# Kernel tuning notes

Measured on AMD Instinct MI355X. Metric: run time of the kernel, lower is better.

The kernel has to match this reference:

```python
import jax, jax.numpy as jnp
from jax import lax
import numpy as np

N, T, PD, TD, F, E, GB = 2048, 256, 5, 5, 128, 65536, 5


def _lstm_layer(x, Wih, Whh, bih, bhh):
    # x: [B, T, D] -> [B, T, H], torch LSTM gate order (i, f, g, o)
    B = x.shape[0]
    H = Whh.shape[1]
    b = bih + bhh

    def step(carry, xt):
        h, c = carry
        gates = xt @ Wih.T + h @ Whh.T + b
        i, f, g, o = jnp.split(gates, 4, axis=-1)
        c = jax.nn.sigmoid(f) * c + jax.nn.sigmoid(i) * jnp.tanh(g)
        h = jax.nn.sigmoid(o) * jnp.tanh(c)
        return (h, c), h

    h0 = jnp.zeros((B, H), x.dtype)
    _, hs = lax.scan(step, (h0, h0), jnp.swapaxes(x, 0, 1))
    return jnp.swapaxes(hs, 0, 1)


def _attention(x, W1, b1, W2, b2):
    # Fused prefix (cumulative causal) softmax attention.
    # Original loops over t computing softmax(scores[:, :t+1]); here:
    # ctx[t] = cumsum(e * x)[t] / cumsum(e)[t] with a global max shift
    # (softmax is shift-invariant, so this equals the per-prefix softmax).
    s = (jnp.tanh(x @ W1.T + b1) @ W2.T + b2)[..., 0]  # [B, T]
    e = jnp.exp(s - jnp.max(s, axis=1, keepdims=True))  # [B, T]
    num = jnp.cumsum(e[..., None] * x, axis=1)          # [B, T, D]
    den = jnp.cumsum(e, axis=1)[..., None]              # [B, T, 1]
    return jnp.sum(num / den, axis=1)                   # [B, D]


def _gcn(x, W, b, edge_index, edge_weight):
    # PyG GCNConv with normalize=True: add self-loops (w=1), symmetric norm.
    n = x.shape[0]
    loop = jnp.arange(n)
    row = jnp.concatenate([edge_index[0], loop])
    col = jnp.concatenate([edge_index[1], loop])
    w = jnp.concatenate([edge_weight, jnp.ones((n,), edge_weight.dtype)])
    deg = jax.ops.segment_sum(w, col, num_segments=n)
    dinv = jnp.where(deg > 0, deg ** -0.5, 0.0)
    norm = dinv[row] * w * dinv[col]
    h = x @ W.T
    out = jax.ops.segment_sum(norm[:, None] * h[row], col, num_segments=n)
    return out + b


def _forward(price, global_trend, p_weights, t_weights,
             lp_Wih0, lp_Whh0, lp_bih0, lp_bhh0, lp_Wih1, lp_Whh1, lp_bih1, lp_bhh1,
             lt_Wih0, lt_Whh0, lt_bih0, lt_bhh0, lt_Wih1, lt_Whh1, lt_bih1, lt_bhh1,
             ap_W1, ap_b1, ap_W2, ap_b2, at_W1, at_b1, at_W2, at_b2,
             gp1_W, gp1_b, gp2_W, gp2_b, gt1_W, gt1_b, gt2_W, gt2_b,
             mlp_W, mlp_b, p_edge_index, t_edge_index):
    x = _lstm_layer(price, lp_Wih0, lp_Whh0, lp_bih0, lp_bhh0)
    x = _lstm_layer(x, lp_Wih1, lp_Whh1, lp_bih1, lp_bhh1)
    x = _attention(x, ap_W1, ap_b1, ap_W2, ap_b2)            # [N, F]
    g = _lstm_layer(global_trend, lt_Wih0, lt_Whh0, lt_bih0, lt_bhh0)
    g = _lstm_layer(g, lt_Wih1, lt_Whh1, lt_bih1, lt_bhh1)
    g = _attention(g, at_W1, at_b1, at_W2, at_b2)            # [GB, F]
    pg = _gcn(x, gp1_W, gp1_b, p_edge_index, p_weights)
    pg = _gcn(pg, gp2_W, gp2_b, p_edge_index, p_weights)     # [N, F]
    # NOTE: original feeds x (not g) into the trend graph convs.
    tg = _gcn(x, gt1_W, gt1_b, t_edge_index, t_weights)
    tg = _gcn(tg, gt2_W, gt2_b, t_edge_index, t_weights)     # [N, F]
    trend = tg @ g.T                                         # [N, GB]
    feat = jnp.concatenate([pg, trend], axis=1)              # [N, F+GB]
    return jax.nn.sigmoid(feat @ mlp_W.T + mlp_b)            # [N, 1]


def setup_inputs() -> dict:
    key = jax.random.key(0)
    ks = iter(jax.random.split(key, 64))
    nrm = lambda shape, s=0.05: jax.random.normal(next(ks), shape, jnp.float32) * s
    inp = {}
    inp['price'] = jax.random.normal(next(ks), (N, T, PD), jnp.float32)
    inp['global_trend'] = jax.random.normal(next(ks), (GB, T, TD), jnp.float32)
    inp['p_edge_index'] = jax.random.randint(next(ks), (2, E), 0, N)
    inp['p_weights'] = jax.random.uniform(next(ks), (E,), jnp.float32)
    inp['t_edge_index'] = jax.random.randint(next(ks), (2, E), 0, N)
    inp['t_weights'] = jax.random.uniform(next(ks), (E,), jnp.float32)
    for pre, d in (('lp', PD), ('lt', TD)):
        inp[pre + '_Wih0'] = nrm((4 * F, d)); inp[pre + '_Whh0'] = nrm((4 * F, F))
        inp[pre + '_bih0'] = nrm((4 * F,));   inp[pre + '_bhh0'] = nrm((4 * F,))
        inp[pre + '_Wih1'] = nrm((4 * F, F)); inp[pre + '_Whh1'] = nrm((4 * F, F))
        inp[pre + '_bih1'] = nrm((4 * F,));   inp[pre + '_bhh1'] = nrm((4 * F,))
    for pre in ('ap', 'at'):
        inp[pre + '_W1'] = nrm((F, F)); inp[pre + '_b1'] = jnp.zeros((F,), jnp.float32)
        inp[pre + '_W2'] = nrm((1, F)); inp[pre + '_b2'] = jnp.zeros((1,), jnp.float32)
    for pre in ('gp', 'gt'):
        inp[pre + '1_W'] = nrm((16, F)); inp[pre + '1_b'] = jnp.zeros((16,), jnp.float32)
        inp[pre + '2_W'] = nrm((F, 16)); inp[pre + '2_b'] = jnp.zeros((F,), jnp.float32)
    inp['mlp_W'] = nrm((1, F + GB)); inp['mlp_b'] = jnp.zeros((1,), jnp.float32)
    return inp


def reference(price, global_trend, p_edge_index, p_weights, t_edge_index, t_weights,
              lp_Wih0, lp_Whh0, lp_bih0, lp_bhh0, lp_Wih1, lp_Whh1, lp_bih1, lp_bhh1,
              lt_Wih0, lt_Whh0, lt_bih0, lt_bhh0, lt_Wih1, lt_Whh1, lt_bih1, lt_bhh1,
              ap_W1, ap_b1, ap_W2, ap_b2, at_W1, at_b1, at_W2, at_b2,
              gp1_W, gp1_b, gp2_W, gp2_b, gt1_W, gt1_b, gt2_W, gt2_b,
              mlp_W, mlp_b):
    return _forward(price, global_trend, p_weights, t_weights,
                    lp_Wih0, lp_Whh0, lp_bih0, lp_bhh0, lp_Wih1, lp_Whh1, lp_bih1, lp_bhh1,
                    lt_Wih0, lt_Whh0, lt_bih0, lt_bhh0, lt_Wih1, lt_Whh1, lt_bih1, lt_bhh1,
                    ap_W1, ap_b1, ap_W2, ap_b2, at_W1, at_b1, at_W2, at_b2,
                    gp1_W, gp1_b, gp2_W, gp2_b, gt1_W, gt1_b, gt2_W, gt2_b,
                    mlp_W, mlp_b, p_edge_index, t_edge_index)
```

## Files before the change

kernel.cpp:

```cpp
#include <hip/hip_runtime.h>
#include <hip/hip_bf16.h>
#include <cstddef>

#define TT    256
#define NROW  2048
#define GBN   5
#define EDG   65536

using f32x4  = __attribute__((ext_vector_type(4))) float;
using bf16x8 = __attribute__((ext_vector_type(8))) short;

__device__ __forceinline__ void pinv(bf16x8& x) { asm volatile("" : "+v"(x)); }

__device__ __forceinline__ void barrier_lgkm() {
  asm volatile("s_waitcnt lgkmcnt(0)" ::: "memory");
  __builtin_amdgcn_s_barrier();
}

__device__ __forceinline__ float exp2fa(float x) { float r; asm("v_exp_f32 %0, %1" : "=v"(r) : "v"(x)); return r; }
__device__ __forceinline__ float rcpfa(float x)  { float r; asm("v_rcp_f32 %0, %1" : "=v"(r) : "v"(x)); return r; }
#define L2E 1.4426950408889634f
__device__ __forceinline__ float sigf(float x) { return rcpfa(1.0f + exp2fa(x * -L2E)); }
__device__ __forceinline__ float tanh_fast(float x) {
  float t = exp2fa(x * (-2.0f * L2E));
  return (1.0f - t) * rcpfa(1.0f + t);
}

enum : int {
  XBUF   = 425984,
  GBUFO  = 688128,
  DINVP  = 688768,
  DINVT  = 690816,
  H16    = 692864,
  PG1    = 725632,
  H128   = 758400,
  PGB    = 1020544,
  TG1    = 1282688,
  TGB    = 1315456,
  WS_END = 1577600
};

enum : int {
  N_P0   = 0,
  N_P1I  = 65536,
  N_P1H  = 131072,
  N_PA   = 196608,
  N_T0   = 212992,
  N_T1I  = 278528,
  N_T1H  = 344064,
  N_TA   = 409600
};

enum : long long {
  C0S_O   = 1577600,
  C1S_O   = 1841792,
  H1IMG_O = 2105984,
  SMST_O  = 2370176,
  NUMS_O  = 2374304,
  ACCOS_O = 2638496,
  H0S_O   = 2902688
};

struct SmemPipe {
  ushort a[2][2048];
  ushort b[2][2048];
  float  x[2560];
  float  s[2][8][16];
};

__global__ void k_pack(const float* __restrict__ Wa, const float* __restrict__ Wb,
                       int K1, int K2, int NT, int KS, ushort* __restrict__ dst) {
  int t = blockIdx.x * blockDim.x + threadIdx.x;
  int total = KS * NT * 2 * 64;
  if (t >= total) return;
  int lane = t & 63;
  int part = (t >> 6) & 1;
  int rest = t >> 7;
  int nt = rest % NT, kk = rest / NT;
  int j = nt * 16 + (lane & 15);
  int kbase = kk * 32 + (lane >> 4) * 8;
  bf16x8 o;
  #pragma unroll
  for (int e = 0; e < 8; ++e) {
    int k = kbase + e;
    float x = (k < K1) ? Wa[(size_t)j * K1 + k] : Wb[(size_t)j * K2 + (k - K1)];
    __hip_bfloat16 hi = __float2bfloat16(x);
    ushort u;
    if (part == 0) {
      u = *(ushort*)&hi;
    } else {
      float lo = x - __bfloat162float(hi);
      __hip_bfloat16 lob = __float2bfloat16(lo);
      u = *(ushort*)&lob;
    }
    o[e] = (short)u;
  }
  ((bf16x8*)dst)[t] = o;
}

__global__ void k_zero(float* __restrict__ p, int n) {
  int i = blockIdx.x * blockDim.x + threadIdx.x;
  if (i < n) p[i] = 0.0f;
}
__global__ void k_fill1(float* __restrict__ p, int n) {
  int i = blockIdx.x * blockDim.x + threadIdx.x;
  if (i < n) p[i] = 1.0f;
}
__global__ void k_deg(const int* __restrict__ col, const float* __restrict__ w,
                      float* __restrict__ deg, int n) {
  int i = blockIdx.x * blockDim.x + threadIdx.x;
  if (i < n) atomicAdd(&deg[col[i]], w[i]);
}
__global__ void k_dinv(float* __restrict__ deg, int n) {
  int i = blockIdx.x * blockDim.x + threadIdx.x;
  if (i < n) deg[i] = rsqrtf(deg[i]);
}

__device__ static void lstm0_body(
    SmemPipe* sm, int b,
    const float* __restrict__ price, const float* __restrict__ gtrend,
    const float* __restrict__ ws_ro, ushort* __restrict__ h0S, float* __restrict__ c0S,
    const float* __restrict__ Wih0p, const float* __restrict__ bi0p, const float* __restrict__ bh0p,
    const float* __restrict__ Wih0t, const float* __restrict__ bi0t, const float* __restrict__ bh0t,
    int nPrice, int t0, int TCp, int first)
{
  const int tid = threadIdx.x;
  const int w = tid >> 6, l = tid & 63;
  const int lq = l >> 4, lr = l & 15;
  const int rb = lq * 4;
  const int kcol = w * 16 + lr;
  const bool isP = b < nPrice;
  const int R = isP ? 16 : GBN;
  const float* seq = isP ? (price + (size_t)b * 16 * (TT * 5)) : gtrend;
  const ushort* S0 = (const ushort*)(ws_ro + (isP ? N_P0 : N_T0));
  const float* Wih0 = isP ? Wih0p : Wih0t;
  const float* bi0 = isP ? bi0p : bi0t;
  const float* bh0 = isP ? bh0p : bh0t;

  auto h0hi = sm->a;
  auto h0lo = sm->b;
  float* xsa = sm->x;

  bf16x8 wh[4][4], wl[4][4];
  #pragma unroll
  for (int kk = 0; kk < 4; ++kk)
    #pragma unroll
    for (int g = 0; g < 4; ++g) {
      int blk = (kk * 32 + (w + 8 * g)) * 2;
      wh[kk][g] = ((const bf16x8*)S0)[(blk + 0) * 64 + l];
      wl[kk][g] = ((const bf16x8*)S0)[(blk + 1) * 64 + l];
      pinv(wh[kk][g]); pinv(wl[kk][g]);
    }
  float wih0r[4][5], bg0[4];
  #pragma unroll
  for (int g = 0; g < 4; ++g) {
    int j = kcol + 128 * g;
    bg0[g] = bi0[j] + bh0[j];
    #pragma unroll
    for (int k = 0; k < 5; ++k) wih0r[g][k] = Wih0[j * 5 + k];
  }

  const size_t bstr = (size_t)b * (size_t)TCp * 4096;
  float c0[4] = {0, 0, 0, 0};

  for (int i = tid; i < TCp * 80; i += 512) {
    int tl = i / 80, rem = i % 80, r = rem / 5, k = rem % 5;
    xsa[tl * 80 + rem] = (r < R) ? seq[(size_t)r * (TT * 5) + (size_t)(t0 + tl) * 5 + k] : 0.0f;
  }
  if (first) {
    for (int i = tid; i < 2048; i += 512) { h0hi[0][i] = 0; h0lo[0][i] = 0; }
  } else {
    const size_t lb = bstr + (size_t)(TCp - 1) * 4096;
    *(uint2*)&h0hi[0][4 * tid] = *(const uint2*)&h0S[lb + 4 * tid];
    *(uint2*)&h0lo[0][4 * tid] = *(const uint2*)&h0S[lb + 2048 + 4 * tid];
    #pragma unroll
    for (int reg = 0; reg < 4; ++reg)
      c0[reg] = c0S[(size_t)b * 2048 + (size_t)(rb + reg) * 128 + kcol];
  }
  __syncthreads();

  const int kkhi = (kcol >> 3) & 3;
  const int eo = kcol & 7;
  const int b0w = rb + 16 * kkhi;
  const int kkw = kcol >> 5;
  int wro[4];
  #pragma unroll
  for (int reg = 0; reg < 4; ++reg) wro[reg] = kkw * 512 + (b0w + (reg ^ lq)) * 8 + eo;
  const int rdo = (l ^ ((l >> 2) & 3)) * 8;

  int cur = 0;
  for (int tl = 0; tl < TCp; ++tl) {
    const int nxt = cur ^ 1;
    if (tl > 0) {
      *(uint2*)&h0S[bstr + (size_t)(tl - 1) * 4096 + 4 * tid] = *(const uint2*)&h0hi[cur][4 * tid];
      *(uint2*)&h0S[bstr + (size_t)(tl - 1) * 4096 + 2048 + 4 * tid] = *(const uint2*)&h0lo[cur][4 * tid];
    }

    f32x4 acc[4];
    #pragma unroll
    for (int g = 0; g < 4; ++g) acc[g] = (f32x4){bg0[g], bg0[g], bg0[g], bg0[g]};
    #pragma unroll
    for (int k = 0; k < 5; ++k) {
      float xv[4];
      #pragma unroll
      for (int reg = 0; reg < 4; ++reg) xv[reg] = xsa[tl * 80 + (rb + reg) * 5 + k];
      #pragma unroll
      for (int g = 0; g < 4; ++g)
        #pragma unroll
        for (int reg = 0; reg < 4; ++reg)
          acc[g][reg] = fmaf(xv[reg], wih0r[g][k], acc[g][reg]);
    }
    #pragma unroll
    for (int kk = 0; kk < 4; ++kk) {
      bf16x8 ah = *(const bf16x8*)&h0hi[cur][kk * 512 + rdo];
      bf16x8 al = *(const bf16x8*)&h0lo[cur][kk * 512 + rdo];
      #pragma unroll
      for (int g = 0; g < 4; ++g) {
        acc[g] = __builtin_amdgcn_mfma_f32_16x16x32_bf16(ah, wh[kk][g], acc[g], 0, 0, 0);
        acc[g] = __builtin_amdgcn_mfma_f32_16x16x32_bf16(al, wh[kk][g], acc[g], 0, 0, 0);
        acc[g] = __builtin_amdgcn_mfma_f32_16x16x32_bf16(ah, wl[kk][g], acc[g], 0, 0, 0);
      }
    }
    #pragma unroll
    for (int reg = 0; reg < 4; ++reg) {
      float gi = acc[0][reg], gf = acc[1][reg], gg = acc[2][reg], go = acc[3][reg];
      float c = sigf(gf) * c0[reg] + sigf(gi) * tanh_fast(gg);
      c0[reg] = c;
      float h = sigf(go) * tanh_fast(c);
      __hip_bfloat16 hb = __float2bfloat16(h);
      float lo = h - __bfloat162float(hb);
      __hip_bfloat16 lb = __float2bfloat16(lo);
      h0hi[nxt][wro[reg]] = *(ushort*)&hb;
      h0lo[nxt][wro[reg]] = *(ushort*)&lb;
    }
    barrier_lgkm();
    cur = nxt;
  }
  *(uint2*)&h0S[bstr + (size_t)(TCp - 1) * 4096 + 4 * tid] = *(const uint2*)&h0hi[cur][4 * tid];
  *(uint2*)&h0S[bstr + (size_t)(TCp - 1) * 4096 + 2048 + 4 * tid] = *(const uint2*)&h0lo[cur][4 * tid];

  #pragma unroll
  for (int reg = 0; reg < 4; ++reg)
    c0S[(size_t)b * 2048 + (size_t)(rb + reg) * 128 + kcol] = c0[reg];
}

__device__ static void lstm1_body(
    SmemPipe* sm, int b,
    const float* __restrict__ pre1, const float* __restrict__ ws_ro,
    float* __restrict__ xout, float* __restrict__ gout,
    float* __restrict__ c1S, ushort* __restrict__ h1imgS, float* __restrict__ smS,
    float* __restrict__ numS, float* __restrict__ accOS,
    const float* __restrict__ apB1, const float* __restrict__ apW2, const float* __restrict__ apB2,
    const float* __restrict__ atB1, const float* __restrict__ atW2, const float* __restrict__ atB2,
    int nPrice, int TCp, int first)
{
  const int tid = threadIdx.x;
  const int w = tid >> 6, l = tid & 63;
  const int lq = l >> 4, lr = l & 15;
  const int rb = lq * 4;
  const int kcol = w * 16 + lr;
  const bool isP = b < nPrice;
  const int R = isP ? 16 : GBN;
  const ushort* S1H = (const ushort*)(ws_ro + (isP ? N_P1H : N_T1H));
  const ushort* SA  = (const ushort*)(ws_ro + (isP ? N_PA : N_TA));
  const float* b1ap = isP ? apB1 : atB1;
  const float* w2p  = isP ? apW2 : atW2;
  const float  b2v  = isP ? apB2[0] : atB2[0];

  auto h1hi = sm->a;
  auto h1lo = sm->b;
  auto sbuf = sm->s;

  bf16x8 hh[4][4], hl[4][4];
  #pragma unroll
  for (int kk = 0; kk < 4; ++kk)
    #pragma unroll
    for (int g = 0; g < 4; ++g) {
      int blk = (kk * 32 + (w + 8 * g)) * 2;
      hh[kk][g] = ((const bf16x8*)S1H)[(blk + 0) * 64 + l];
      hl[kk][g] = ((const bf16x8*)S1H)[(blk + 1) * 64 + l];
      pinv(hh[kk][g]); pinv(hl[kk][g]);
    }
  bf16x8 wa[4], wal[4];
  #pragma unroll
  for (int kk = 0; kk < 4; ++kk) {
    wa[kk]  = ((const bf16x8*)SA)[((kk * 8 + w) * 2 + 0) * 64 + l];
    wal[kk] = ((const bf16x8*)SA)[((kk * 8 + w) * 2 + 1) * 64 + l];
    pinv(wa[kk]); pinv(wal[kk]);
  }
  const float w2r = w2p[kcol], b1ar = b1ap[kcol];

  float c1[4] = {0, 0, 0, 0}, h1r[4] = {0, 0, 0, 0}, h1r_prev[4];
  float num[4] = {0, 0, 0, 0}, accO[4] = {0, 0, 0, 0};
  float m_run[4], den_r[4];

  if (first) {
    for (int i = tid; i < 2048; i += 512) { h1hi[0][i] = 0; h1lo[0][i] = 0; }
    #pragma unroll
    for (int reg = 0; reg < 4; ++reg) { m_run[reg] = -1e30f; den_r[reg] = 0.0f; }
  } else {
    const size_t ib = (size_t)b * 4096;
    *(uint2*)&h1hi[0][4 * tid] = *(const uint2*)&h1imgS[ib + 4 * tid];
    *(uint2*)&h1lo[0][4 * tid] = *(const uint2*)&h1imgS[ib + 2048 + 4 * tid];
    const size_t sb = (size_t)b * 2048;
    #pragma unroll
    for (int reg = 0; reg < 4; ++reg) {
      size_t o = sb + (size_t)(rb + reg) * 128 + kcol;
      c1[reg] = c1S[o];
      num[reg] = numS[o];
      accO[reg] = accOS[o];
      m_run[reg] = smS[(size_t)b * 32 + (size_t)(rb + reg) * 2];
      den_r[reg] = smS[(size_t)b * 32 + (size_t)(rb + reg) * 2 + 1];
    }
  }
  __syncthreads();

  const int kkhi = (kcol >> 3) & 3;
  const int eo = kcol & 7;
  const int b0w = rb + 16 * kkhi;
  const int kkw = kcol >> 5;
  int wro[4];
  #pragma unroll
  for (int reg = 0; reg < 4; ++reg) wro[reg] = kkw * 512 + (b0w + (reg ^ lq)) * 8 + eo;
  const int rdo = (l ^ ((l >> 2) & 3)) * 8;

  const float* pbase = pre1 + (size_t)b * TCp * 8192 + (size_t)tid * 16;

  f32x4 pnext[4];
  #pragma unroll
  for (int g = 0; g < 4; ++g) pnext[g] = *(const f32x4*)&pbase[g * 4];

  int cur = 0;
  for (int tl = 0; tl < TCp; ++tl) {
    const int nxt = cur ^ 1;
    f32x4 acc[4];
    #pragma unroll
    for (int g = 0; g < 4; ++g) acc[g] = pnext[g];
    if (tl + 1 < TCp) {
      #pragma unroll
      for (int g = 0; g < 4; ++g)
        pnext[g] = *(const f32x4*)&pbase[(size_t)(tl + 1) * 8192 + g * 4];
    }

    #pragma unroll
    for (int kk = 0; kk < 4; ++kk) {
      bf16x8 ah = *(const bf16x8*)&h1hi[cur][kk * 512 + rdo];
      bf16x8 al = *(const bf16x8*)&h1lo[cur][kk * 512 + rdo];
      #pragma unroll
      for (int g = 0; g < 4; ++g) {
        acc[g] = __builtin_amdgcn_mfma_f32_16x16x32_bf16(ah, hh[kk][g], acc[g], 0, 0, 0);
        acc[g] = __builtin_amdgcn_mfma_f32_16x16x32_bf16(al, hh[kk][g], acc[g], 0, 0, 0);
        acc[g] = __builtin_amdgcn_mfma_f32_16x16x32_bf16(ah, hl[kk][g], acc[g], 0, 0, 0);
      }
    }
    #pragma unroll
    for (int reg = 0; reg < 4; ++reg) {
      h1r_prev[reg] = h1r[reg];
      float gi = acc[0][reg], gf = acc[1][reg], gg = acc[2][reg], go = acc[3][reg];
      float c = sigf(gf) * c1[reg] + sigf(gi) * tanh_fast(gg);
      c1[reg] = c;
      float h = sigf(go) * tanh_fast(c);
      h1r[reg] = h;
      __hip_bfloat16 hb = __float2bfloat16(h);
      float lo = h - __bfloat162float(hb);
      __hip_bfloat16 lb = __float2bfloat16(lo);
      h1hi[nxt][wro[reg]] = *(ushort*)&hb;
      h1lo[nxt][wro[reg]] = *(ushort*)&lb;
    }
    barrier_lgkm();

    if (tl > 0) {
      const int pb = (tl - 1) & 1;
      #pragma unroll
      for (int reg = 0; reg < 4; ++reg) {
        float s = b2v;
        #pragma unroll
        for (int ww = 0; ww < 8; ++ww) s += sbuf[pb][ww][rb + reg];
        float m0 = m_run[reg];
        float nm = fmaxf(m0, s);
        float e = exp2fa((s - nm) * L2E), sc = exp2fa((m0 - nm) * L2E);
        float d = den_r[reg] * sc + e;
        m_run[reg] = nm; den_r[reg] = d;
        num[reg] = num[reg] * sc + e * h1r_prev[reg];
        accO[reg] = fmaf(num[reg], rcpfa(d), accO[reg]);
      }
    }

    f32x4 aa = (f32x4){b1ar, b1ar, b1ar, b1ar};
    #pragma unroll
    for (int kk = 0; kk < 4; ++kk) {
      bf16x8 ah = *(const bf16x8*)&h1hi[nxt][kk * 512 + rdo];
      bf16x8 al = *(const bf16x8*)&h1lo[nxt][kk * 512 + rdo];
      aa = __builtin_amdgcn_mfma_f32_16x16x32_bf16(ah, wa[kk], aa, 0, 0, 0);
      aa = __builtin_amdgcn_mfma_f32_16x16x32_bf16(al, wa[kk], aa, 0, 0, 0);
      aa = __builtin_amdgcn_mfma_f32_16x16x32_bf16(ah, wal[kk], aa, 0, 0, 0);
    }
    float p[4];
    #pragma unroll
    for (int reg = 0; reg < 4; ++reg) p[reg] = tanh_fast(aa[reg]) * w2r;
    #pragma unroll
    for (int m = 1; m < 16; m <<= 1) {
      #pragma unroll
      for (int reg = 0; reg < 4; ++reg) p[reg] += __shfl_xor(p[reg], m);
    }
    if (lr == 0) {
      #pragma unroll
      for (int reg = 0; reg < 4; ++reg) sbuf[tl & 1][w][rb + reg] = p[reg];
    }
    cur = nxt;
  }
  barrier_lgkm();
  {
    const int pb = (TCp - 1) & 1;
    #pragma unroll
    for (int reg = 0; reg < 4; ++reg) {
      float s = b2v;
      #pragma unroll
      for (int ww = 0; ww < 8; ++ww) s += sbuf[pb][ww][rb + reg];
      float m0 = m_run[reg];
      float nm = fmaxf(m0, s);
      float e = exp2fa((s - nm) * L2E), sc = exp2fa((m0 - nm) * L2E);
      float d = den_r[reg] * sc + e;
      m_run[reg] = nm; den_r[reg] = d;
      num[reg] = num[reg] * sc + e * h1r[reg];
      accO[reg] = fmaf(num[reg], rcpfa(d), accO[reg]);
    }
  }

  {
    const size_t ib = (size_t)b * 4096;
    *(uint2*)&h1imgS[ib + 4 * tid] = *(const uint2*)&h1hi[cur][4 * tid];
    *(uint2*)&h1imgS[ib + 2048 + 4 * tid] = *(const uint2*)&h1lo[cur][4 * tid];
    const size_t sb = (size_t)b * 2048;
    #pragma unroll
    for (int reg = 0; reg < 4; ++reg) {
      size_t o = sb + (size_t)(rb + reg) * 128 + kcol;
      c1S[o] = c1[reg];
      numS[o] = num[reg];
      accOS[o] = accO[reg];
    }
    if (w == 0 && lr == 0) {
      #pragma unroll
      for (int reg = 0; reg < 4; ++reg) {
        smS[(size_t)b * 32 + (size_t)(rb + reg) * 2] = m_run[reg];
        smS[(size_t)b * 32 + (size_t)(rb + reg) * 2 + 1] = den_r[reg];
      }
    }
  }

  float* dstx = isP ? (xout + (size_t)b * 16 * 128) : gout;
  #pragma unroll
  for (int reg = 0; reg < 4; ++reg) {
    int r = rb + reg;
    if (r < R) dstx[(size_t)r * 128 + kcol] = accO[reg];
  }
}

__global__ __launch_bounds__(512, 2) void k_pipe(
    const float* __restrict__ price, const float* __restrict__ gtrend,
    const float* __restrict__ ws_ro, ushort* __restrict__ h0S, float* __restrict__ c0S,
    const float* __restrict__ Wih0p, const float* __restrict__ bi0p, const float* __restrict__ bh0p,
    const float* __restrict__ Wih0t, const float* __restrict__ bi0t, const float* __restrict__ bh0t,
    const float* __restrict__ pre1,
    float* __restrict__ xout, float* __restrict__ gout,
    float* __restrict__ c1S, ushort* __restrict__ h1imgS, float* __restrict__ smS,
    float* __restrict__ numS, float* __restrict__ accOS,
    const float* __restrict__ apB1, const float* __restrict__ apW2, const float* __restrict__ apB2,
    const float* __restrict__ atB1, const float* __restrict__ atW2, const float* __restrict__ atB2,
    int nPrice, int t0A, int TCp, int firstA, int firstB, int doA, int doB)
{
  __shared__ SmemPipe sm;
  const int bid = blockIdx.x;
  if (bid < 129) {
    if (doA)
      lstm0_body(&sm, bid, price, gtrend, ws_ro, h0S, c0S,
                 Wih0p, bi0p, bh0p, Wih0t, bi0t, bh0t, nPrice, t0A, TCp, firstA);
  } else {
    if (doB)
      lstm1_body(&sm, bid - 129, pre1, ws_ro, xout, gout,
                 c1S, h1imgS, smS, numS, accOS,
                 apB1, apW2, apB2, atB1, atW2, atB2, nPrice, TCp, firstB);
  }
}

__global__ __launch_bounds__(512, 2) void k_pre1(
    const ushort* __restrict__ h0S, const float* __restrict__ ws_ro,
    float* __restrict__ pre1,
    const float* __restrict__ bi1p, const float* __restrict__ bh1p,
    const float* __restrict__ bi1t, const float* __restrict__ bh1t,
    int nPrice, int TCp, int nsub)
{
  const int b = blockIdx.x / nsub, sub = blockIdx.x % nsub;
  const int tid = threadIdx.x;
  const int w = tid >> 6, l = tid & 63;
  const int lr = l & 15;
  const int kcol = w * 16 + lr;
  const bool isP = b < nPrice;
  const ushort* S1I = (const ushort*)(ws_ro + (isP ? N_P1I : N_T1I));
  const float* bi1 = isP ? bi1p : bi1t;
  const float* bh1 = isP ? bh1p : bh1t;
  float bg1[4];
  #pragma unroll
  for (int g = 0; g < 4; ++g) bg1[g] = bi1[kcol + 128 * g] + bh1[kcol + 128 * g];
  const int rdo = (l ^ ((l >> 2) & 3)) * 8;
  const size_t bstr = (size_t)b * (size_t)TCp * 4096;
  const int t0 = sub * 4;

  f32x4 acc[4][4];
  #pragma unroll
  for (int ts = 0; ts < 4; ++ts)
    #pragma unroll
    for (int g = 0; g < 4; ++g) acc[ts][g] = (f32x4){bg1[g], bg1[g], bg1[g], bg1[g]};

  #pragma unroll
  for (int kk = 0; kk < 4; ++kk) {
    bf16x8 bh_[4], bl_[4];
    #pragma unroll
    for (int g = 0; g < 4; ++g) {
      int blk = (kk * 32 + (w + 8 * g)) * 2;
      bh_[g] = ((const bf16x8*)S1I)[(blk + 0) * 64 + l];
      bl_[g] = ((const bf16x8*)S1I)[(blk + 1) * 64 + l];
    }
    #pragma unroll
    for (int ts = 0; ts < 4; ++ts) {
      const size_t tb = bstr + (size_t)(t0 + ts) * 4096 + kk * 512 + rdo;
      bf16x8 ah = *(const bf16x8*)&h0S[tb];
      bf16x8 al = *(const bf16x8*)&h0S[tb + 2048];
      #pragma unroll
      for (int g = 0; g < 4; ++g) {
        acc[ts][g] = __builtin_amdgcn_mfma_f32_16x16x32_bf16(ah, bh_[g], acc[ts][g], 0, 0, 0);
        acc[ts][g] = __builtin_amdgcn_mfma_f32_16x16x32_bf16(al, bh_[g], acc[ts][g], 0, 0, 0);
        acc[ts][g] = __builtin_amdgcn_mfma_f32_16x16x32_bf16(ah, bl_[g], acc[ts][g], 0, 0, 0);
      }
    }
  }
  #pragma unroll
  for (int ts = 0; ts < 4; ++ts)
    #pragma unroll
    for (int g = 0; g < 4; ++g)
      *(f32x4*)&pre1[((size_t)b * TCp + (t0 + ts)) * 8192 + (size_t)tid * 16 + g * 4] = acc[ts][g];
}

__global__ void k_lin(const float* __restrict__ x, const float* __restrict__ W,
                      float* __restrict__ h, int M, int K, int n) {
  int i = blockIdx.x * blockDim.x + threadIdx.x;
  if (i >= n) return;
  int r = i / M, m = i % M;
  const float* xr = x + (size_t)r * K;
  const float* wm = W + (size_t)m * K;
  float a = 0.f;
  for (int k = 0; k < K; ++k) a = fmaf(xr[k], wm[k], a);
  h[i] = a;
}

__global__ void k_scatter(const int* __restrict__ rowi, const int* __restrict__ coli,
                          const float* __restrict__ w, const float* __restrict__ dinv,
                          const float* __restrict__ h, float* __restrict__ outp,
                          int M, long long n) {
  long long i = (long long)blockIdx.x * blockDim.x + threadIdx.x;
  if (i >= n) return;
  int e = (int)(i / M), f = (int)(i % M);
  int rs = rowi[e], cd = coli[e];
  float nrm = dinv[rs] * w[e] * dinv[cd];
  atomicAdd(&outp[(size_t)cd * M + f], nrm * h[(size_t)rs * M + f]);
}

__global__ void k_gcn_fin(float* __restrict__ io, const float* __restrict__ h,
                          const float* __restrict__ dinv, const float* __restrict__ b,
                          int M, int n) {
  int i = blockIdx.x * blockDim.x + threadIdx.x;
  if (i >= n) return;
  int v = i / M, f = i % M;
  float dv = dinv[v];
  io[i] += dv * dv * h[i] + b[f];
}

__global__ __launch_bounds__(256) void k_final(const float* __restrict__ pg, const float* __restrict__ tg,
                                               const float* __restrict__ g, const float* __restrict__ mw,
                                               const float* __restrict__ mb, float* __restrict__ outp) {
  int wv = threadIdx.x >> 6, ln = threadIdx.x & 63;
  int r = blockIdx.x * 4 + wv;
  const float* pr = pg + (size_t)r * 128;
  const float* tr = tg + (size_t)r * 128;
  float pa = pr[ln] * mw[ln] + pr[ln + 64] * mw[ln + 64];
  float t0 = tr[ln], t1 = tr[ln + 64];
  float s[GBN];
  #pragma unroll
  for (int gb = 0; gb < GBN; ++gb)
    s[gb] = g[gb * 128 + ln] * t0 + g[gb * 128 + 64 + ln] * t1;
  #pragma unroll
  for (int o = 32; o > 0; o >>= 1) {
    pa += __shfl_down(pa, o);
    #pragma unroll
    for (int gb = 0; gb < GBN; ++gb) s[gb] += __shfl_down(s[gb], o);
  }
  if (ln == 0) {
    float lg = pa + mb[0];
    #pragma unroll
    for (int gb = 0; gb < GBN; ++gb) lg = fmaf(s[gb], mw[128 + gb], lg);
    outp[r] = 1.0f / (1.0f + __expf(-lg));
  }
}

static inline int gdiv(long long n) { return (int)((n + 255) / 256); }

extern "C" void kernel_launch(void* const* d_in, const int* in_sizes, int n_in,
                              void* d_out, int out_size, void* d_ws, size_t ws_size,
                              hipStream_t stream) {
  const float* price  = (const float*)d_in[0];
  const float* gtrend = (const float*)d_in[1];
  const int*   p_ei   = (const int*)d_in[2];
  const float* p_w    = (const float*)d_in[3];
  const int*   t_ei   = (const int*)d_in[4];
  const float* t_w    = (const float*)d_in[5];
  const float* lpWih0 = (const float*)d_in[6];
  const float* lpWhh0 = (const float*)d_in[7];
  const float* lpBih0 = (const float*)d_in[8];
  const float* lpBhh0 = (const float*)d_in[9];
  const float* lpWih1 = (const float*)d_in[10];
  const float* lpWhh1 = (const float*)d_in[11];
  const float* lpBih1 = (const float*)d_in[12];
  const float* lpBhh1 = (const float*)d_in[13];
  const float* ltWih0 = (const float*)d_in[14];
  const float* ltWhh0 = (const float*)d_in[15];
  const float* ltBih0 = (const float*)d_in[16];
  const float* ltBhh0 = (const float*)d_in[17];
  const float* ltWih1 = (const float*)d_in[18];
  const float* ltWhh1 = (const float*)d_in[19];
  const float* ltBih1 = (const float*)d_in[20];
  const float* ltBhh1 = (const float*)d_in[21];
  const float* apW1 = (const float*)d_in[22];
  const float* apB1 = (const float*)d_in[23];
  const float* apW2 = (const float*)d_in[24];
  const float* apB2 = (const float*)d_in[25];
  const float* atW1 = (const float*)d_in[26];
  const float* atB1 = (const float*)d_in[27];
  const float* atW2 = (const float*)d_in[28];
  const float* atB2 = (const float*)d_in[29];
  const float* gp1W = (const float*)d_in[30];
  const float* gp1b = (const float*)d_in[31];
  const float* gp2W = (const float*)d_in[32];
  const float* gp2b = (const float*)d_in[33];
  const float* gt1W = (const float*)d_in[34];
  const float* gt1b = (const float*)d_in[35];
  const float* gt2W = (const float*)d_in[36];
  const float* gt2b = (const float*)d_in[37];
  const float* mlpW = (const float*)d_in[38];
  const float* mlpb = (const float*)d_in[39];

  float* ws = (float*)d_ws;
  float* outp = (float*)d_out;
  if (ws_size < (size_t)WS_END * sizeof(float)) return;

  int TC = 0;
  for (int cand = 32; cand >= 8; cand >>= 1) {
    unsigned long long need = ((unsigned long long)H0S_O + 129ULL * cand * (2048ULL + 8192ULL)) * 4ULL;
    if ((unsigned long long)ws_size >= need) { TC = cand; break; }
  }
  if (TC == 0) return;

  k_pack<<<gdiv(16384), 256, 0, stream>>>(lpWhh0, lpWhh0, 128, 128, 32, 4, (ushort*)(ws + N_P0));
  k_pack<<<gdiv(16384), 256, 0, stream>>>(lpWih1, lpWih1, 128, 128, 32, 4, (ushort*)(ws + N_P1I));
  k_pack<<<gdiv(16384), 256, 0, stream>>>(lpWhh1, lpWhh1, 128, 128, 32, 4, (ushort*)(ws + N_P1H));
  k_pack<<<gdiv(4096),  256, 0, stream>>>(apW1,   apW1,   128, 128,  8, 4, (ushort*)(ws + N_PA));
  k_pack<<<gdiv(16384), 256, 0, stream>>>(ltWhh0, ltWhh0, 128, 128, 32, 4, (ushort*)(ws + N_T0));
  k_pack<<<gdiv(16384), 256, 0, stream>>>(ltWih1, ltWih1, 128, 128, 32, 4, (ushort*)(ws + N_T1I));
  k_pack<<<gdiv(16384), 256, 0, stream>>>(ltWhh1, ltWhh1, 128, 128, 32, 4, (ushort*)(ws + N_T1H));
  k_pack<<<gdiv(4096),  256, 0, stream>>>(atW1,   atW1,   128, 128,  8, 4, (ushort*)(ws + N_TA));

  k_fill1<<<gdiv(NROW), 256, 0, stream>>>(ws + DINVP, NROW);
  k_deg<<<gdiv(EDG), 256, 0, stream>>>(p_ei + EDG, p_w, ws + DINVP, EDG);
  k_dinv<<<gdiv(NROW), 256, 0, stream>>>(ws + DINVP, NROW);
  k_fill1<<<gdiv(NROW), 256, 0, stream>>>(ws + DINVT, NROW);
  k_deg<<<gdiv(EDG), 256, 0, stream>>>(t_ei + EDG, t_w, ws + DINVT, EDG);
  k_dinv<<<gdiv(NROW), 256, 0, stream>>>(ws + DINVT, NROW);

  ushort* h0S = (ushort*)(ws + H0S_O);
  float*  pre1 = ws + H0S_O + (long long)129 * TC * 2048;
  {
    const int CH = TT / TC;
    const int nsub = TC / 4;
    for (int c = 0; c < CH; ++c) {
      k_pipe<<<258, 512, 0, stream>>>(price, gtrend, ws, h0S, ws + C0S_O,
                                      lpWih0, lpBih0, lpBhh0,
                                      ltWih0, ltBih0, ltBhh0,
                                      pre1, ws + XBUF, ws + GBUFO,
                                      ws + C1S_O, (ushort*)(ws + H1IMG_O), ws + SMST_O,
                                      ws + NUMS_O, ws + ACCOS_O,
                                      apB1, apW2, apB2, atB1, atW2, atB2,
                                      128, c * TC, TC,
                                      c == 0 ? 1 : 0,
                                      c == 1 ? 1 : 0,
                                      1, c > 0 ? 1 : 0);
      k_pre1<<<129 * nsub, 512, 0, stream>>>(h0S, ws, pre1,
                                             lpBih1, lpBhh1, ltBih1, ltBhh1,
                                             128, TC, nsub);
    }
    k_pipe<<<258, 512, 0, stream>>>(price, gtrend, ws, h0S, ws + C0S_O,
                                    lpWih0, lpBih0, lpBhh0,
                                    ltWih0, ltBih0, ltBhh0,
                                    pre1, ws + XBUF, ws + GBUFO,
                                    ws + C1S_O, (ushort*)(ws + H1IMG_O), ws + SMST_O,
                                    ws + NUMS_O, ws + ACCOS_O,
                                    apB1, apW2, apB2, atB1, atW2, atB2,
                                    128, 0, TC,
                                    0, CH == 1 ? 1 : 0,
                                    0, 1);
  }

  k_lin<<<gdiv(NROW * 16), 256, 0, stream>>>(ws + XBUF, gp1W, ws + H16, 16, 128, NROW * 16);
  k_zero<<<gdiv(NROW * 16), 256, 0, stream>>>(ws + PG1, NROW * 16);
  k_scatter<<<gdiv((long long)EDG * 16), 256, 0, stream>>>(p_ei, p_ei + EDG, p_w, ws + DINVP,
                                                           ws + H16, ws + PG1, 16, (long long)EDG * 16);
  k_gcn_fin<<<gdiv(NROW * 16), 256, 0, stream>>>(ws + PG1, ws + H16, ws + DINVP, gp1b, 16, NROW * 16);
  k_lin<<<gdiv(NROW * 128), 256, 0, stream>>>(ws + PG1, gp2W, ws + H128, 128, 16, NROW * 128);
  k_zero<<<gdiv(NROW * 128), 256, 0, stream>>>(ws + PGB, NROW * 128);
  k_scatter<<<gdiv((long long)EDG * 128), 256, 0, stream>>>(p_ei, p_ei + EDG, p_w, ws + DINVP,
                                                            ws + H128, ws + PGB, 128, (long long)EDG * 128);
  k_gcn_fin<<<gdiv(NROW * 128), 256, 0, stream>>>(ws + PGB, ws + H128, ws + DINVP, gp2b, 128, NROW * 128);

  k_lin<<<gdiv(NROW * 16), 256, 0, stream>>>(ws + XBUF, gt1W, ws + H16, 16, 128, NROW * 16);
  k_zero<<<gdiv(NROW * 16), 256, 0, stream>>>(ws + TG1, NROW * 16);
  k_scatter<<<gdiv((long long)EDG * 16), 256, 0, stream>>>(t_ei, t_ei + EDG, t_w, ws + DINVT,
                                                           ws + H16, ws + TG1, 16, (long long)EDG * 16);
  k_gcn_fin<<<gdiv(NROW * 16), 256, 0, stream>>>(ws + TG1, ws + H16, ws + DINVT, gt1b, 16, NROW * 16);
  k_lin<<<gdiv(NROW * 128), 256, 0, stream>>>(ws + TG1, gt2W, ws + H128, 128, 16, NROW * 128);
  k_zero<<<gdiv(NROW * 128), 256, 0, stream>>>(ws + TGB, NROW * 128);
  k_scatter<<<gdiv((long long)EDG * 128), 256, 0, stream>>>(t_ei, t_ei + EDG, t_w, ws + DINVT,
                                                            ws + H128, ws + TGB, 128, (long long)EDG * 128);
  k_gcn_fin<<<gdiv(NROW * 128), 256, 0, stream>>>(ws + TGB, ws + H128, ws + DINVT, gt2b, 128, NROW * 128);

  k_final<<<512, 256, 0, stream>>>(ws + PGB, ws + TGB, ws + GBUFO, mlpW, mlpb, outp);
}
```

Before: 2.367 ms.

## Process two layer-1 LSTM tiles per workgroup to share weights and halve blocks

Each layer-1 LSTM workgroup now handles two 16-row batch tiles at once, reusing the register-resident recurrent and attention weights and interleaving two independent MFMA chains per step. The launch shrinks from 258 to 194 blocks. The trend tile sits alone in its block with a dummy second tile. Shared memory is enlarged and padded, likely to limit occupancy to one block per CU, at the cost of higher register pressure and duplicated work for the trend block.

Result: slower. 3.701 ms (+56.3%).

```diff
diff --git a/kernel.cpp b/kernel.cpp
--- a/kernel.cpp
+++ b/kernel.cpp
@@ -61,11 +61,12 @@
   H0S_O   = 2902688
 };
 
-struct SmemPipe {
-  ushort a[2][2048];
-  ushort b[2][2048];
+struct __align__(16) SmemPipe {
+  ushort a[2][4096];
+  ushort b[2][4096];
   float  x[2560];
-  float  s[2][8][16];
+  float  s[2][8][32];
+  float  pad[10240];
 };
 
 __global__ void k_pack(const float* __restrict__ Wa, const float* __restrict__ Wb,
@@ -245,22 +246,24 @@
 }
 
 __device__ static void lstm1_body(
-    SmemPipe* sm, int b,
+    SmemPipe* sm, int b32,
     const float* __restrict__ pre1, const float* __restrict__ ws_ro,
     float* __restrict__ xout, float* __restrict__ gout,
     float* __restrict__ c1S, ushort* __restrict__ h1imgS, float* __restrict__ smS,
     float* __restrict__ numS, float* __restrict__ accOS,
     const float* __restrict__ apB1, const float* __restrict__ apW2, const float* __restrict__ apB2,
     const float* __restrict__ atB1, const float* __restrict__ atW2, const float* __restrict__ atB2,
-    int nPrice, int TCp, int first)
+    int TCp, int first)
 {
   const int tid = threadIdx.x;
   const int w = tid >> 6, l = tid & 63;
   const int lq = l >> 4, lr = l & 15;
   const int rb = lq * 4;
   const int kcol = w * 16 + lr;
-  const bool isP = b < nPrice;
-  const int R = isP ? 16 : GBN;
+  const bool isP = b32 < 64;
+  const bool t1on = isP;
+  const int bb0 = isP ? 2 * b32 : 128;
+  const int bb1 = isP ? 2 * b32 + 1 : 128;
   const ushort* S1H = (const ushort*)(ws_ro + (isP ? N_P1H : N_T1H));
   const ushort* SA  = (const ushort*)(ws_ro + (isP ? N_PA : N_TA));
   const float* b1ap = isP ? apB1 : atB1;
@@ -290,27 +293,46 @@
   }
   const float w2r = w2p[kcol], b1ar = b1ap[kcol];
 
-  float c1[4] = {0, 0, 0, 0}, h1r[4] = {0, 0, 0, 0}, h1r_prev[4];
-  float num[4] = {0, 0, 0, 0}, accO[4] = {0, 0, 0, 0};
-  float m_run[4], den_r[4];
+  float c1[2][4] = {{0,0,0,0},{0,0,0,0}}, h1r[2][4] = {{0,0,0,0},{0,0,0,0}}, h1rp[2][4];
+  float num[2][4] = {{0,0,0,0},{0,0,0,0}}, accO[2][4] = {{0,0,0,0},{0,0,0,0}};
+  float m_run[2][4], den_r[2][4];
+  #pragma unroll
+  for (int t = 0; t < 2; ++t)
+    #pragma unroll
+    for (int reg = 0; reg < 4; ++reg) { m_run[t][reg] = -1e30f; den_r[t][reg] = 0.0f; }
 
   if (first) {
-    for (int i = tid; i < 2048; i += 512) { h1hi[0][i] = 0; h1lo[0][i] = 0; }
-    #pragma unroll
-    for (int reg = 0; reg < 4; ++reg) { m_run[reg] = -1e30f; den_r[reg] = 0.0f; }
+    for (int i = tid; i < 4096; i += 512) { h1hi[0][i] = 0; h1lo[0][i] = 0; }
   } else {
-    const size_t ib = (size_t)b * 4096;
-    *(uint2*)&h1hi[0][4 * tid] = *(const uint2*)&h1imgS[ib + 4 * tid];
-    *(uint2*)&h1lo[0][4 * tid] = *(const uint2*)&h1imgS[ib + 2048 + 4 * tid];
-    const size_t sb = (size_t)b * 2048;
-    #pragma unroll
-    for (int reg = 0; reg < 4; ++reg) {
-      size_t o = sb + (size_t)(rb + reg) * 128 + kcol;
-      c1[reg] = c1S[o];
-      num[reg] = numS[o];
-      accO[reg] = accOS[o];
-      m_run[reg] = smS[(size_t)b * 32 + (size_t)(rb + reg) * 2];
-      den_r[reg] = smS[(size_t)b * 32 + (size_t)(rb + reg) * 2 + 1];
+    {
+      const size_t ib = (size_t)bb0 * 4096;
+      *(uint2*)&h1hi[0][4 * tid] = *(const uint2*)&h1imgS[ib + 4 * tid];
+      *(uint2*)&h1lo[0][4 * tid] = *(const uint2*)&h1imgS[ib + 2048 + 4 * tid];
+      const size_t sb = (size_t)bb0 * 2048;
+      #pragma unroll
+      for (int reg = 0; reg < 4; ++reg) {
+        size_t o = sb + (size_t)(rb + reg) * 128 + kcol;
+        c1[0][reg] = c1S[o];
+        num[0][reg] = numS[o];
+        accO[0][reg] = accOS[o];
+        m_run[0][reg] = smS[(size_t)bb0 * 32 + (size_t)(rb + reg) * 2];
+        den_r[0][reg] = smS[(size_t)bb0 * 32 + (size_t)(rb + reg) * 2 + 1];
+      }
+    }
+    if (t1on) {
+      const size_t ib = (size_t)bb1 * 4096;
+      *(uint2*)&h1hi[0][2048 + 4 * tid] = *(const uint2*)&h1imgS[ib + 4 * tid];
+      *(uint2*)&h1lo[0][2048 + 4 * tid] = *(const uint2*)&h1imgS[ib + 2048 + 4 * tid];
+      const size_t sb = (size_t)bb1 * 2048;
+      #pragma unroll
+      for (int reg = 0; reg < 4; ++reg) {
+        size_t o = sb + (size_t)(rb + reg) * 128 + kcol;
+        c1[1][reg] = c1S[o];
+        num[1][reg] = numS[o];
+        accO[1][reg] = accOS[o];
+        m_run[1][reg] = smS[(size_t)bb1 * 32 + (size_t)(rb + reg) * 2];
+        den_r[1][reg] = smS[(size_t)bb1 * 32 + (size_t)(rb + reg) * 2 + 1];
+      }
     }
   }
   __syncthreads();
@@ -324,135 +346,172 @@
   for (int reg = 0; reg < 4; ++reg) wro[reg] = kkw * 512 + (b0w + (reg ^ lq)) * 8 + eo;
   const int rdo = (l ^ ((l >> 2) & 3)) * 8;
 
-  const float* pbase = pre1 + (size_t)b * TCp * 8192 + (size_t)tid * 16;
-
-  f32x4 pnext[4];
-  #pragma unroll
-  for (int g = 0; g < 4; ++g) pnext[g] = *(const f32x4*)&pbase[g * 4];
+  const float* pbA = pre1 + (size_t)bb0 * TCp * 8192 + (size_t)tid * 16;
+  const float* pbB = pre1 + (size_t)bb1 * TCp * 8192 + (size_t)tid * 16;
+
+  f32x4 pnA[4], pnB[4];
+  #pragma unroll
+  for (int g = 0; g < 4; ++g) { pnA[g] = *(const f32x4*)&pbA[g * 4]; pnB[g] = *(const f32x4*)&pbB[g * 4]; }
 
   int cur = 0;
   for (int tl = 0; tl < TCp; ++tl) {
     const int nxt = cur ^ 1;
-    f32x4 acc[4];
-    #pragma unroll
-    for (int g = 0; g < 4; ++g) acc[g] = pnext[g];
+    f32x4 acc[2][4];
+    #pragma unroll
+    for (int g = 0; g < 4; ++g) { acc[0][g] = pnA[g]; acc[1][g] = pnB[g]; }
     if (tl + 1 < TCp) {
       #pragma unroll
-      for (int g = 0; g < 4; ++g)
-        pnext[g] = *(const f32x4*)&pbase[(size_t)(tl + 1) * 8192 + g * 4];
+      for (int g = 0; g < 4; ++g) {
+        pnA[g] = *(const f32x4*)&pbA[(size_t)(tl + 1) * 8192 + g * 4];
+        pnB[g] = *(const f32x4*)&pbB[(size_t)(tl + 1) * 8192 + g * 4];
+      }
     }
 
     #pragma unroll
     for (int kk = 0; kk < 4; ++kk) {
-      bf16x8 ah = *(const bf16x8*)&h1hi[cur][kk * 512 + rdo];
-      bf16x8 al = *(const bf16x8*)&h1lo[cur][kk * 512 + rdo];
+      bf16x8 ah0 = *(const bf16x8*)&h1hi[cur][kk * 512 + rdo];
+      bf16x8 al0 = *(const bf16x8*)&h1lo[cur][kk * 512 + rdo];
+      bf16x8 ah1 = *(const bf16x8*)&h1hi[cur][2048 + kk * 512 + rdo];
+      bf16x8 al1 = *(const bf16x8*)&h1lo[cur][2048 + kk * 512 + rdo];
       #pragma unroll
       for (int g = 0; g < 4; ++g) {
-        acc[g] = __builtin_amdgcn_mfma_f32_16x16x32_bf16(ah, hh[kk][g], acc[g], 0, 0, 0);
-        acc[g] = __builtin_amdgcn_mfma_f32_16x16x32_bf16(al, hh[kk][g], acc[g], 0, 0, 0);
-        acc[g] = __builtin_amdgcn_mfma_f32_16x16x32_bf16(ah, hl[kk][g], acc[g], 0, 0, 0);
-      }
-    }
-    #pragma unroll
-    for (int reg = 0; reg < 4; ++reg) {
-      h1r_prev[reg] = h1r[reg];
-      float gi = acc[0][reg], gf = acc[1][reg], gg = acc[2][reg], go = acc[3][reg];
-      float c = sigf(gf) * c1[reg] + sigf(gi) * tanh_fast(gg);
-      c1[reg] = c;
-      float h = sigf(go) * tanh_fast(c);
-      h1r[reg] = h;
-      __hip_bfloat16 hb = __float2bfloat16(h);
-      float lo = h - __bfloat162float(hb);
-      __hip_bfloat16 lb = __float2bfloat16(lo);
-      h1hi[nxt][wro[reg]] = *(ushort*)&hb;
-      h1lo[nxt][wro[reg]] = *(ushort*)&lb;
-    }
+        acc[0][g] = __builtin_amdgcn_mfma_f32_16x16x32_bf16(ah0, hh[kk][g], acc[0][g], 0, 0, 0);
+        acc[0][g] = __builtin_amdgcn_mfma_f32_16x16x32_bf16(al0, hh[kk][g], acc[0][g], 0, 0, 0);
+        acc[0][g] = __builtin_amdgcn_mfma_f32_16x16x32_bf16(ah0, hl[kk][g], acc[0][g], 0, 0, 0);
+        acc[1][g] = __builtin_amdgcn_mfma_f32_16x16x32_bf16(ah1, hh[kk][g], acc[1][g], 0, 0, 0);
+        acc[1][g] = __builtin_amdgcn_mfma_f32_16x16x32_bf16(al1, hh[kk][g], acc[1][g], 0, 0, 0);
+        acc[1][g] = __builtin_amdgcn_mfma_f32_16x16x32_bf16(ah1, hl[kk][g], acc[1][g], 0, 0, 0);
+      }
+    }
+    #pragma unroll
+    for (int t = 0; t < 2; ++t)
+      #pragma unroll
+      for (int reg = 0; reg < 4; ++reg) {
+        h1rp[t][reg] = h1r[t][reg];
+        float gi = acc[t][0][reg], gf = acc[t][1][reg], gg = acc[t][2][reg], go = acc[t][3][reg];
+        float c = sigf(gf) * c1[t][reg] + sigf(gi) * tanh_fast(gg);
+        c1[t][reg] = c;
+        float h = sigf(go) * tanh_fast(c);
+        h1r[t][reg] = h;
+        __hip_bfloat16 hb = __float2bfloat16(h);
+        float lo = h - __bfloat162float(hb);
+        __hip_bfloat16 lb = __float2bfloat16(lo);
+        h1hi[nxt][t * 2048 + wro[reg]] = *(ushort*)&hb;
+        h1lo[nxt][t * 2048 + wro[reg]] = *(ushort*)&lb;
+      }
     barrier_lgkm();
 
     if (tl > 0) {
       const int pb = (tl - 1) & 1;
+      #pragma unroll
+      for (int t = 0; t < 2; ++t)
+        #pragma unroll
+        for (int reg = 0; reg < 4; ++reg) {
+          float s = b2v;
+          #pragma unroll
+          for (int ww = 0; ww < 8; ++ww) s += sbuf[pb][ww][t * 16 + rb + reg];
+          float m0 = m_run[t][reg];
+          float nm = fmaxf(m0, s);
+          float e = exp2fa((s - nm) * L2E), sc = exp2fa((m0 - nm) * L2E);
+          float d = den_r[t][reg] * sc + e;
+          m_run[t][reg] = nm; den_r[t][reg] = d;
+          num[t][reg] = num[t][reg] * sc + e * h1rp[t][reg];
+          accO[t][reg] = fmaf(num[t][reg], rcpfa(d), accO[t][reg]);
+        }
+    }
+
+    f32x4 aa[2];
+    aa[0] = (f32x4){b1ar, b1ar, b1ar, b1ar};
+    aa[1] = aa[0];
+    #pragma unroll
+    for (int kk = 0; kk < 4; ++kk) {
+      bf16x8 ah0 = *(const bf16x8*)&h1hi[nxt][kk * 512 + rdo];
+      bf16x8 al0 = *(const bf16x8*)&h1lo[nxt][kk * 512 + rdo];
+      bf16x8 ah1 = *(const bf16x8*)&h1hi[nxt][2048 + kk * 512 + rdo];
+      bf16x8 al1 = *(const bf16x8*)&h1lo[nxt][2048 + kk * 512 + rdo];
+      aa[0] = __builtin_amdgcn_mfma_f32_16x16x32_bf16(ah0, wa[kk], aa[0], 0, 0, 0);
+      aa[0] = __builtin_amdgcn_mfma_f32_16x16x32_bf16(al0, wa[kk], aa[0], 0, 0, 0);
+      aa[0] = __builtin_amdgcn_mfma_f32_16x16x32_bf16(ah0, wal[kk], aa[0], 0, 0, 0);
+      aa[1] = __builtin_amdgcn_mfma_f32_16x16x32_bf16(ah1, wa[kk], aa[1], 0, 0, 0);
+      aa[1] = __builtin_amdgcn_mfma_f32_16x16x32_bf16(al1, wa[kk], aa[1], 0, 0, 0);
+      aa[1] = __builtin_amdgcn_mfma_f32_16x16x32_bf16(ah1, wal[kk], aa[1], 0, 0, 0);
+    }
+    float p[2][4];
+    #pragma unroll
+    for (int t = 0; t < 2; ++t)
+      #pragma unroll
+      for (int reg = 0; reg < 4; ++reg) p[t][reg] = tanh_fast(aa[t][reg]) * w2r;
+    #pragma unroll
+    for (int m = 1; m < 16; m <<= 1) {
+      #pragma unroll
+      for (int t = 0; t < 2; ++t)
+        #pragma unroll
+        for (int reg = 0; reg < 4; ++reg) p[t][reg] += __shfl_xor(p[t][reg], m);
+    }
+    if (lr == 0) {
+      #pragma unroll
+      for (int t = 0; t < 2; ++t)
+        #pragma unroll
+        for (int reg = 0; reg < 4; ++reg) sbuf[tl & 1][w][t * 16 + rb + reg] = p[t][reg];
+    }
+    cur = nxt;
+  }
+  barrier_lgkm();
+  {
+    const int pb = (TCp - 1) & 1;
+    #pragma unroll
+    for (int t = 0; t < 2; ++t)
       #pragma unroll
       for (int reg = 0; reg < 4; ++reg) {
         float s = b2v;
         #pragma unroll
-        for (int ww = 0; ww < 8; ++ww) s += sbuf[pb][ww][rb + reg];
-        float m0 = m_run[reg];
+        for (int ww = 0; ww < 8; ++ww) s += sbuf[pb][ww][t * 16 + rb + reg];
+        float m0 = m_run[t][reg];
         float nm = fmaxf(m0, s);
         float e = exp2fa((s - nm) * L2E), sc = exp2fa((m0 - nm) * L2E);
-        float d = den_r[reg] * sc + e;
-        m_run[reg] = nm; den_r[reg] = d;
-        num[reg] = num[reg] * sc + e * h1r_prev[reg];
-        accO[reg] = fmaf(num[reg], rcpfa(d), accO[reg]);
-      }
-    }
-
-    f32x4 aa = (f32x4){b1ar, b1ar, b1ar, b1ar};
-    #pragma unroll
-    for (int kk = 0; kk < 4; ++kk) {
-      bf16x8 ah = *(const bf16x8*)&h1hi[nxt][kk * 512 + rdo];
-      bf16x8 al = *(const bf16x8*)&h1lo[nxt][kk * 512 + rdo];
-      aa = __builtin_amdgcn_mfma_f32_16x16x32_bf16(ah, wa[kk], aa, 0, 0, 0);
-      aa = __builtin_amdgcn_mfma_f32_16x16x32_bf16(al, wa[kk], aa, 0, 0, 0);
-      aa = __builtin_amdgcn_mfma_f32_16x16x32_bf16(ah, wal[kk], aa, 0, 0, 0);
-    }
-    float p[4];
-    #pragma unroll
-    for (int reg = 0; reg < 4; ++reg) p[reg] = tanh_fast(aa[reg]) * w2r;
-    #pragma unroll
-    for (int m = 1; m < 16; m <<= 1) {
-      #pragma unroll
-      for (int reg = 0; reg < 4; ++reg) p[reg] += __shfl_xor(p[reg], m);
-    }
-    if (lr == 0) {
-      #pragma unroll
-      for (int reg = 0; reg < 4; ++reg) sbuf[tl & 1][w][rb + reg] = p[reg];
-    }
-    cur = nxt;
-  }
-  barrier_lgkm();
+        float d = den_r[t][reg] * sc + e;
+        m_run[t][reg] = nm; den_r[t][reg] = d;
+        num[t][reg] = num[t][reg] * sc + e * h1r[t][reg];
+        accO[t][reg] = fmaf(num[t][reg], rcpfa(d), accO[t][reg]);
+      }
+  }
+
   {
-    const int pb = (TCp - 1) & 1;
-    #pragma unroll
-    for (int reg = 0; reg < 4; ++reg) {
-      float s = b2v;
-      #pragma unroll
-      for (int ww = 0; ww < 8; ++ww) s += sbuf[pb][ww][rb + reg];
-      float m0 = m_run[reg];
-      float nm = fmaxf(m0, s);
-      float e = exp2fa((s - nm) * L2E), sc = exp2fa((m0 - nm) * L2E);
-      float d = den_r[reg] * sc + e;
-      m_run[reg] = nm; den_r[reg] = d;
-      num[reg] = num[reg] * sc + e * h1r[reg];
-      accO[reg] = fmaf(num[reg], rcpfa(d), accO[reg]);
-    }
-  }
-
-  {
-    const size_t ib = (size_t)b * 4096;
-    *(uint2*)&h1imgS[ib + 4 * tid] = *(const uint2*)&h1hi[cur][4 * tid];
-    *(uint2*)&h1imgS[ib + 2048 + 4 * tid] = *(const uint2*)&h1lo[cur][4 * tid];
-    const size_t sb = (size_t)b * 2048;
-    #pragma unroll
-    for (int reg = 0; reg < 4; ++reg) {
-      size_t o = sb + (size_t)(rb + reg) * 128 + kcol;
-      c1S[o] = c1[reg];
-      numS[o] = num[reg];
-      accOS[o] = accO[reg];
-    }
-    if (w == 0 && lr == 0) {
+    const size_t ib0 = (size_t)bb0 * 4096;
+    *(uint2*)&h1imgS[ib0 + 4 * tid] = *(const uint2*)&h1hi[cur][4 * tid];
+    *(uint2*)&h1imgS[ib0 + 2048 + 4 * tid] = *(const uint2*)&h1lo[cur][4 * tid];
+    if (t1on) {
+      const size_t ib1 = (size_t)bb1 * 4096;
+      *(uint2*)&h1imgS[ib1 + 4 * tid] = *(const uint2*)&h1hi[cur][2048 + 4 * tid];
+      *(uint2*)&h1imgS[ib1 + 2048 + 4 * tid] = *(const uint2*)&h1lo[cur][2048 + 4 * tid];
+    }
+    #pragma unroll
+    for (int t = 0; t < 2; ++t) {
+      if (t == 1 && !t1on) continue;
+      const int bbt = t == 0 ? bb0 : bb1;
+      const size_t sb = (size_t)bbt * 2048;
       #pragma unroll
       for (int reg = 0; reg < 4; ++reg) {
-        smS[(size_t)b * 32 + (size_t)(rb + reg) * 2] = m_run[reg];
-        smS[(size_t)b * 32 + (size_t)(rb + reg) * 2 + 1] = den_r[reg];
-      }
-    }
-  }
-
-  float* dstx = isP ? (xout + (size_t)b * 16 * 128) : gout;
-  #pragma unroll
-  for (int reg = 0; reg < 4; ++reg) {
-    int r = rb + reg;
-    if (r < R) dstx[(size_t)r * 128 + kcol] = accO[reg];
+        size_t o = sb + (size_t)(rb + reg) * 128 + kcol;
+        c1S[o] = c1[t][reg];
+        numS[o] = num[t][reg];
+        accOS[o] = accO[t][reg];
+      }
+      if (w == 0 && lr == 0) {
+        #pragma unroll
+        for (int reg = 0; reg < 4; ++reg) {
+          smS[(size_t)bbt * 32 + (size_t)(rb + reg) * 2] = m_run[t][reg];
+          smS[(size_t)bbt * 32 + (size_t)(rb + reg) * 2 + 1] = den_r[t][reg];
+        }
+      }
+      const int Rt = isP ? 16 : GBN;
+      float* dstx = isP ? (xout + (size_t)bbt * 16 * 128) : gout;
+      #pragma unroll
+      for (int reg = 0; reg < 4; ++reg) {
+        int r = rb + reg;
+        if (r < Rt) dstx[(size_t)r * 128 + kcol] = accO[t][reg];
+      }
+    }
   }
 }
 
@@ -467,19 +526,19 @@
     float* __restrict__ numS, float* __restrict__ accOS,
     const float* __restrict__ apB1, const float* __restrict__ apW2, const float* __restrict__ apB2,
     const float* __restrict__ atB1, const float* __restrict__ atW2, const float* __restrict__ atB2,
-    int nPrice, int t0A, int TCp, int firstA, int firstB, int doA, int doB)
+    int t0A, int TCp, int firstA, int firstB, int doA, int doB)
 {
   __shared__ SmemPipe sm;
   const int bid = blockIdx.x;
   if (bid < 129) {
     if (doA)
       lstm0_body(&sm, bid, price, gtrend, ws_ro, h0S, c0S,
-                 Wih0p, bi0p, bh0p, Wih0t, bi0t, bh0t, nPrice, t0A, TCp, firstA);
+                 Wih0p, bi0p, bh0p, Wih0t, bi0t, bh0t, 128, t0A, TCp, firstA);
   } else {
     if (doB)
       lstm1_body(&sm, bid - 129, pre1, ws_ro, xout, gout,
                  c1S, h1imgS, smS, numS, accOS,
-                 apB1, apW2, apB2, atB1, atW2, atB2, nPrice, TCp, firstB);
+                 apB1, apW2, apB2, atB1, atW2, atB2, TCp, firstB);
   }
 }
 
@@ -681,31 +740,28 @@
     const int CH = TT / TC;
     const int nsub = TC / 4;
     for (int c = 0; c < CH; ++c) {
-      k_pipe<<<258, 512, 0, stream>>>(price, gtrend, ws, h0S, ws + C0S_O,
+      k_pipe<<<194, 512, 0, stream>>>(price, gtrend, ws, h0S, ws + C0S_O,
                                       lpWih0, lpBih0, lpBhh0,
                                       ltWih0, ltBih0, ltBhh0,
                                       pre1, ws + XBUF, ws + GBUFO,
                                       ws + C1S_O, (ushort*)(ws + H1IMG_O), ws + SMST_O,
                                       ws + NUMS_O, ws + ACCOS_O,
                                       apB1, apW2, apB2, atB1, atW2, atB2,
-                                      128, c * TC, TC,
-                                      c == 0 ? 1 : 0,
-                                      c == 1 ? 1 : 0,
+                                      c * TC, TC,
+                                      c == 0 ? 1 : 0, c == 1 ? 1 : 0,
                                       1, c > 0 ? 1 : 0);
       k_pre1<<<129 * nsub, 512, 0, stream>>>(h0S, ws, pre1,
                                              lpBih1, lpBhh1, ltBih1, ltBhh1,
                                              128, TC, nsub);
     }
-    k_pipe<<<258, 512, 0, stream>>>(price, gtrend, ws, h0S, ws + C0S_O,
+    k_pipe<<<194, 512, 0, stream>>>(price, gtrend, ws, h0S, ws + C0S_O,
                                     lpWih0, lpBih0, lpBhh0,
                                     ltWih0, ltBih0, ltBhh0,
                                     pre1, ws + XBUF, ws + GBUFO,
                                     ws + C1S_O, (ushort*)(ws + H1IMG_O), ws + SMST_O,
                                     ws + NUMS_O, ws + ACCOS_O,
                                     apB1, apW2, apB2, atB1, atW2, atB2,
-                                    128, 0, TC,
-                                    0, CH == 1 ? 1 : 0,
-                                    0, 1);
+                                    0, TC, 0, CH == 1 ? 1 : 0, 0, 1);
   }
 
   k_lin<<<gdiv(NROW * 16), 256, 0, stream>>>(ws + XBUF, gp1W, ws + H16, 16, 128, NROW * 16);
```
